# Kernel optimization log

Hardware: AMD Instinct MI355X
Metric: run time of the kernel (lower is better)

Reference implementation:

```python
import jax, jax.numpy as jnp
import numpy as np

DIM = 48
HEADS = 4
DIM_HEAD = 16
WS = 800  # window_size
INNER = HEADS * DIM_HEAD  # 64
SCALE = DIM_HEAD ** -0.5


def setup_inputs() -> dict:
    key = jax.random.key(0)
    k1, k2, k3, k4, k5 = jax.random.split(key, 5)
    b, n = 4, 6400
    x1 = jax.random.normal(k1, (b, n, DIM), dtype=jnp.float32)
    x2 = jax.random.normal(k2, (b, n, DIM), dtype=jnp.float32)
    # to_qkv: Linear(dim, inner*3, bias=False) -> weight [3*inner, dim] (torch layout)
    Wqkv = jax.random.normal(k3, (3 * INNER, DIM), dtype=jnp.float32) * (DIM ** -0.5)
    # to_out: Linear(inner, dim) with bias (project_out is True since heads=4, dim_head=16 != dim)
    Wout = jax.random.normal(k4, (DIM, INNER), dtype=jnp.float32) * (INNER ** -0.5)
    bout = jax.random.normal(k5, (DIM,), dtype=jnp.float32) * 0.01
    return {"x1": x1, "x2": x2, "Wqkv": Wqkv, "Wout": Wout, "bout": bout}


def _windowed_attn(x, Wqkv):
    # x: [b, n, c] with n divisible by WS -> independent full attention per window
    b, n, c = x.shape
    nw = n // WS
    xw = x.reshape(b, nw, WS, c)
    # Rearrange 'b n (head dim_head)' with head=HEADS on 3*inner dim, then chunk(3)
    # => layout along last axis is (heads, 3, dim_head)
    qkv = jnp.einsum('bwic,oc->bwio', xw, Wqkv).reshape(b, nw, WS, HEADS, 3, DIM_HEAD)
    q, k, v = qkv[..., 0, :], qkv[..., 1, :], qkv[..., 2, :]  # [b,nw,ws,h,dh]
    dots = jnp.einsum('bwihd,bwjhd->bwhij', q, k) * SCALE      # [b,nw,h,ws,ws]
    attn = jax.nn.softmax(dots, axis=-1)
    out = jnp.einsum('bwhij,bwjhd->bwihd', attn, v)            # [b,nw,ws,h,dh]
    return out.reshape(b, n, INNER)


def reference(x1, x2, Wqkv, Wout, bout):
    o1 = _windowed_attn(x1, Wqkv) @ Wout.T + bout
    o2 = _windowed_attn(x2, Wqkv) @ Wout.T + bout
    return o1 + o2
```

## Files before the change

### kernel.cpp

```cpp
#include <hip/hip_runtime.h>
#include <cstddef>

typedef __attribute__((ext_vector_type(8))) short short8;
typedef __attribute__((ext_vector_type(16))) float f32x16;

#define NB 4
#define NSEQ 6400
#define CDIM 48
#define DHEAD 16
#define WSZ 800
#define NWIN 8
#define INNER 64
#define NROWS 25600
#define NWH 256
#define SCHUNK (WSZ * DHEAD)
#define CHUNK (3 * SCHUNK)
#define QKV_TOTAL (NWH * CHUNK)
#define AO_PER (NROWS * INNER)

static __device__ __forceinline__ uint pkbf(float a, float b) {
  uint r;
  asm("v_cvt_pk_bf16_f32 %0, %1, %2" : "=v"(r) : "v"(a), "v"(b));
  return r;
}
static __device__ __forceinline__ float bf2f(ushort u) {
  return __uint_as_float(((uint)u) << 16);
}

__global__ __launch_bounds__(256) void qkv_mfma(const float* __restrict__ x1,
                                                const float* __restrict__ x2,
                                                const float* __restrict__ Wqkv,
                                                ushort* __restrict__ wsq) {
  const int tid = threadIdx.x;
  const int lane = tid & 63;
  const int wv = tid >> 6;

  __shared__ __align__(16) ushort Wl[18 * 64 * 8];
  __shared__ __align__(16) ushort Obuf[4][6 * 512];

  for (int slot = tid; slot < 1152; slot += 256) {
    const int mtks = slot >> 6, l2 = slot & 63;
    const int mt = mtks / 3, ks = mtks % 3;
    const int o = mt * 32 + (l2 & 31);
    const int c0 = ks * 16 + (l2 >> 5) * 8;
    const float sc = ((o % CDIM) < DHEAD) ? 0.25f : 1.0f;
    const float4* p = reinterpret_cast<const float4*>(Wqkv + (size_t)o * CDIM + c0);
    float4 u = p[0], v = p[1];
    union { uint q[4]; short8 s; } t;
    t.q[0] = pkbf(u.x * sc, u.y * sc); t.q[1] = pkbf(u.z * sc, u.w * sc);
    t.q[2] = pkbf(v.x * sc, v.y * sc); t.q[3] = pkbf(v.z * sc, v.w * sc);
    *reinterpret_cast<short8*>(Wl + (size_t)slot * 8) = t.s;
  }
  __syncthreads();

  const int task = blockIdx.x * 4 + wv;
  const int batch = task >> 1;
  const int mh = task & 1;
  const int e = batch / 800;
  const int rb = (batch % 800) * 32;
  const float* __restrict__ x = e ? x2 : x1;

  const int rl = lane & 31;
  const int lg = lane >> 5;
  const int row = rb + rl;

  short8 bf[3];
#pragma unroll
  for (int ks = 0; ks < 3; ++ks) {
    const float4* p =
        reinterpret_cast<const float4*>(x + (size_t)row * CDIM + ks * 16 + lg * 8);
    float4 u = p[0], v = p[1];
    union { uint q[4]; short8 s; } t;
    t.q[0] = pkbf(u.x, u.y); t.q[1] = pkbf(u.z, u.w);
    t.q[2] = pkbf(v.x, v.y); t.q[3] = pkbf(v.z, v.w);
    bf[ks] = t.s;
  }

  const int b = rb / NSEQ;
  const int i0 = rb % NSEQ;
  const int wi = i0 / WSZ;
  const int iwb = i0 % WSZ;
  const int whb = ((e * NB + b) * NWIN + wi) * 4;

#pragma unroll
  for (int mt = mh * 3; mt < mh * 3 + 3; ++mt) {
    const int obase = mt * 32;
    short8 wf0 = *reinterpret_cast<const short8*>(Wl + ((mt * 3 + 0) * 64 + lane) * 8);
    short8 wf1 = *reinterpret_cast<const short8*>(Wl + ((mt * 3 + 1) * 64 + lane) * 8);
    short8 wf2 = *reinterpret_cast<const short8*>(Wl + ((mt * 3 + 2) * 64 + lane) * 8);

    f32x16 acc;
#pragma unroll
    for (int r = 0; r < 16; ++r) acc[r] = 0.f;
    acc = __builtin_amdgcn_mfma_f32_32x32x16_bf16(wf0, bf[0], acc, 0, 0, 0);
    acc = __builtin_amdgcn_mfma_f32_32x32x16_bf16(wf1, bf[1], acc, 0, 0, 0);
    acc = __builtin_amdgcn_mfma_f32_32x32x16_bf16(wf2, bf[2], acc, 0, 0, 0);

#pragma unroll
    for (int q = 0; q < 4; ++q) {
      const int op = obase + q * 8 + 4 * lg - mh * 96;
      const int g2 = op >> 4;
      const int d0 = op & 15;
      uint2 pk;
      pk.x = pkbf(acc[4 * q + 0], acc[4 * q + 1]);
      pk.y = pkbf(acc[4 * q + 2], acc[4 * q + 3]);
      *reinterpret_cast<uint2*>(&Obuf[wv][g2 * 512 + rl * 16 + d0]) = pk;
    }
  }

#pragma unroll
  for (int g2 = 0; g2 < 6; ++g2) {
    const int g = mh * 6 + g2;
    const int h = g / 3, s = g % 3;
    short8 val = *reinterpret_cast<const short8*>(&Obuf[wv][g2 * 512 + lane * 8]);
    *reinterpret_cast<short8*>(wsq + (size_t)(whb + h) * CHUNK + s * SCHUNK +
                               (size_t)iwb * DHEAD + lane * 8) = val;
  }
}

#define JC 160
#define NCH 5
#define VROW 168
#define VSL (17 * VROW)

__global__ __launch_bounds__(320) void attn_mfma(const ushort* __restrict__ wsq,
                                                 ushort* __restrict__ ao) {
  const int tid = threadIdx.x;
  const int lane = tid & 63;
  const int wv = tid >> 6;
  const int bid = blockIdx.x;
  const int wh = bid & (NWH - 1);
  const int sub = bid >> 8;
  const int qtile = sub * 5 + wv;

  const ushort* __restrict__ Qg = wsq + (size_t)wh * CHUNK;
  const ushort* __restrict__ Kg = Qg + SCHUNK;
  const ushort* __restrict__ Vg = Kg + SCHUNK;

  __shared__ __align__(16) ushort Vs[2][VSL];

  const int vj = tid % 160;
  const int vhalf = tid / 160;

  short8 vreg = *reinterpret_cast<const short8*>(Vg + (size_t)vj * DHEAD + vhalf * 8);

  if (tid < JC) {
    Vs[0][16 * VROW + tid] = 0x3F80;
    Vs[1][16 * VROW + tid] = 0x3F80;
  }

#pragma unroll
  for (int u = 0; u < 8; ++u)
    Vs[0][(vhalf * 8 + u) * VROW + vj] = (ushort)vreg[u];

  vreg = *reinterpret_cast<const short8*>(Vg + (size_t)(JC + vj) * DHEAD + vhalf * 8);

  short8 qf = *reinterpret_cast<const short8*>(
      Qg + (size_t)(qtile * 32 + (lane & 31)) * DHEAD + (lane >> 5) * 8);

  __syncthreads();

  f32x16 sinit;
#pragma unroll
  for (int r = 0; r < 16; ++r) sinit[r] = -8.0f;
  f32x16 accO;
#pragma unroll
  for (int r = 0; r < 16; ++r) accO[r] = 0.f;

  const int n31 = lane & 31;
  const int lg = lane >> 5;
  const int vrow = (n31 <= 16) ? n31 : (n31 & 15);
  const ushort* __restrict__ kfb = Kg + (size_t)n31 * DHEAD + lg * 8;

  for (int ch = 0; ch < NCH; ++ch) {
    const ushort* __restrict__ Vc = Vs[ch & 1];
#pragma unroll
    for (int jl = 0; jl < 5; ++jl) {
      short8 kf = *reinterpret_cast<const short8*>(
          kfb + (size_t)(ch * JC + jl * 32) * DHEAD);
      f32x16 st = __builtin_amdgcn_mfma_f32_32x32x16_bf16(kf, qf, sinit, 0, 0, 0);

      float p[16];
#pragma unroll
      for (int r = 0; r < 16; ++r) p[r] = __expf(st[r]);

      uint x0, x1, y0, y1;
      asm("v_cvt_pk_bf16_f32 %0, %1, %2" : "=v"(x0) : "v"(p[0]), "v"(p[1]));
      asm("v_cvt_pk_bf16_f32 %0, %1, %2" : "=v"(x1) : "v"(p[2]), "v"(p[3]));
      asm("v_cvt_pk_bf16_f32 %0, %1, %2" : "=v"(y0) : "v"(p[4]), "v"(p[5]));
      asm("v_cvt_pk_bf16_f32 %0, %1, %2" : "=v"(y1) : "v"(p[6]), "v"(p[7]));
      asm("v_permlane32_swap_b32 %0, %1" : "+v"(x0), "+v"(y0));
      asm("v_permlane32_swap_b32 %0, %1" : "+v"(x1), "+v"(y1));
      union { uint u[4]; short8 s; } pa0;
      pa0.u[0] = x0; pa0.u[1] = x1; pa0.u[2] = y0; pa0.u[3] = y1;

      uint z0, z1, w0, w1;
      asm("v_cvt_pk_bf16_f32 %0, %1, %2" : "=v"(z0) : "v"(p[8]), "v"(p[9]));
      asm("v_cvt_pk_bf16_f32 %0, %1, %2" : "=v"(z1) : "v"(p[10]), "v"(p[11]));
      asm("v_cvt_pk_bf16_f32 %0, %1, %2" : "=v"(w0) : "v"(p[12]), "v"(p[13]));
      asm("v_cvt_pk_bf16_f32 %0, %1, %2" : "=v"(w1) : "v"(p[14]), "v"(p[15]));
      asm("v_permlane32_swap_b32 %0, %1" : "+v"(z0), "+v"(w0));
      asm("v_permlane32_swap_b32 %0, %1" : "+v"(z1), "+v"(w1));
      union { uint u[4]; short8 s; } pa1;
      pa1.u[0] = z0; pa1.u[1] = z1; pa1.u[2] = w0; pa1.u[3] = w1;

      short8 vf0 = *reinterpret_cast<const short8*>(Vc + vrow * VROW + jl * 32 + lg * 8);
      short8 vf1 = *reinterpret_cast<const short8*>(Vc + vrow * VROW + jl * 32 + 16 + lg * 8);

      accO = __builtin_amdgcn_mfma_f32_32x32x16_bf16(pa0.s, vf0, accO, 0, 0, 0);
      accO = __builtin_amdgcn_mfma_f32_32x32x16_bf16(pa1.s, vf1, accO, 0, 0, 0);
    }
    if (ch + 1 < NCH) {
      __syncthreads();
      const int nxt = (ch + 1) & 1;
#pragma unroll
      for (int u = 0; u < 8; ++u)
        Vs[nxt][(vhalf * 8 + u) * VROW + vj] = (ushort)vreg[u];
      if (ch + 2 < NCH) {
        vreg = *reinterpret_cast<const short8*>(
            Vg + (size_t)((ch + 2) * JC + vj) * DHEAD + vhalf * 8);
      }
      __syncthreads();
    }
  }

  const int h = wh & 3;
  const int w = (wh >> 2) & 7;
  const int b = (wh >> 5) & 3;
  const int e = wh >> 7;
  const size_t rowbase =
      (size_t)e * NROWS + (size_t)b * NSEQ + (size_t)w * WSZ + (size_t)qtile * 32;
  const int src = 16 + 32 * lg;

#pragma unroll
  for (int r = 0; r < 16; ++r) {
    float den = __shfl(accO[r], src);
    if (n31 < 16) {
      int i = (r & 3) + 8 * (r >> 2) + 4 * lg;
      float val = accO[r] * __builtin_amdgcn_rcpf(den);
      ao[(rowbase + i) * INNER + h * DHEAD + n31] = (ushort)pkbf(val, val);
    }
  }
}

#define OSTR 76
__global__ __launch_bounds__(192) void out_proj(const ushort* __restrict__ ao_all,
                                                const float* __restrict__ Wout,
                                                const float* __restrict__ bout,
                                                float* __restrict__ out) {
  const int tid = threadIdx.x;
  const int row0 = blockIdx.x * 64;

  __shared__ float aos[64 * OSTR];

  const ushort* __restrict__ a1 = ao_all;
  const ushort* __restrict__ a2 = ao_all + (size_t)AO_PER;

  for (int idx = tid; idx < 64 * 8; idx += 192) {
    const int r = idx >> 3, c = idx & 7;
    const size_t g = (size_t)(row0 + r) * INNER + c * 8;
    short8 u = *reinterpret_cast<const short8*>(a1 + g);
    short8 v = *reinterpret_cast<const short8*>(a2 + g);
    float4 s0, s1;
    s0.x = bf2f((ushort)u[0]) + bf2f((ushort)v[0]);
    s0.y = bf2f((ushort)u[1]) + bf2f((ushort)v[1]);
    s0.z = bf2f((ushort)u[2]) + bf2f((ushort)v[2]);
    s0.w = bf2f((ushort)u[3]) + bf2f((ushort)v[3]);
    s1.x = bf2f((ushort)u[4]) + bf2f((ushort)v[4]);
    s1.y = bf2f((ushort)u[5]) + bf2f((ushort)v[5]);
    s1.z = bf2f((ushort)u[6]) + bf2f((ushort)v[6]);
    s1.w = bf2f((ushort)u[7]) + bf2f((ushort)v[7]);
    *reinterpret_cast<float4*>(aos + r * OSTR + c * 8) = s0;
    *reinterpret_cast<float4*>(aos + r * OSTR + c * 8 + 4) = s1;
  }

  const int j = tid % 48;
  const int rq = tid / 48;

  float wreg[INNER];
#pragma unroll
  for (int k4 = 0; k4 < 16; ++k4) {
    float4 wv4 = reinterpret_cast<const float4*>(Wout + (size_t)j * INNER)[k4];
    wreg[k4 * 4 + 0] = wv4.x; wreg[k4 * 4 + 1] = wv4.y;
    wreg[k4 * 4 + 2] = wv4.z; wreg[k4 * 4 + 3] = wv4.w;
  }
  const float bj = 2.0f * bout[j];

  __syncthreads();

  for (int r16 = 0; r16 < 16; ++r16) {
    const int r = rq * 16 + r16;
    float a0 = 0.f, a1v = 0.f, a2v = 0.f, a3 = 0.f;
#pragma unroll
    for (int kk = 0; kk < 16; ++kk) {
      const int k4 = (kk + rq * 4) & 15;
      float4 av = *reinterpret_cast<const float4*>(aos + r * OSTR + k4 * 4);
      a0 = fmaf(av.x, wreg[k4 * 4 + 0], a0);
      a1v = fmaf(av.y, wreg[k4 * 4 + 1], a1v);
      a2v = fmaf(av.z, wreg[k4 * 4 + 2], a2v);
      a3 = fmaf(av.w, wreg[k4 * 4 + 3], a3);
    }
    out[(size_t)(row0 + r) * CDIM + j] = (a0 + a1v) + (a2v + a3) + bj;
  }
}

extern "C" void kernel_launch(void* const* d_in, const int* in_sizes, int n_in,
                              void* d_out, int out_size, void* d_ws,
                              size_t ws_size, hipStream_t stream) {
  const float* x1 = (const float*)d_in[0];
  const float* x2 = (const float*)d_in[1];
  const float* Wqkv = (const float*)d_in[2];
  const float* Wout = (const float*)d_in[3];
  const float* bout = (const float*)d_in[4];
  float* out = (float*)d_out;
  ushort* wsq = (ushort*)d_ws;
  ushort* ao = wsq + QKV_TOTAL;

  qkv_mfma<<<dim3(800), dim3(256), 0, stream>>>(x1, x2, Wqkv, wsq);
  attn_mfma<<<dim3(1280), dim3(320), 0, stream>>>(wsq, ao);
  out_proj<<<dim3(400), dim3(192), 0, stream>>>(ao, Wout, bout, out);
}
```

Measured before the change: 65.74 us.

## Rewrite output projection using bf16 MFMA with LDS-staged coalesced stores

Replaces the scalar FP32 FMA output projection with a kernel that converts Wout to bf16 in shared memory and uses 32x32x16 bf16 MFMA instructions. The two attention branches are summed by accumulating both into the same accumulator. Results are staged in LDS per wave and written out with coalesced float4 stores. This aims to cut ALU and LDS cost in the final GEMM, at the price of rounding the weights to bf16.

```diff
diff --git a/kernel.cpp b/kernel.cpp
--- a/kernel.cpp
+++ b/kernel.cpp
@@ -243,64 +243,79 @@
   }
 }
 
-#define OSTR 76
-__global__ __launch_bounds__(192) void out_proj(const ushort* __restrict__ ao_all,
+__global__ __launch_bounds__(256) void out_mfma(const ushort* __restrict__ ao_all,
                                                 const float* __restrict__ Wout,
                                                 const float* __restrict__ bout,
                                                 float* __restrict__ out) {
   const int tid = threadIdx.x;
-  const int row0 = blockIdx.x * 64;
-
-  __shared__ float aos[64 * OSTR];
+  const int lane = tid & 63;
+  const int wv = tid >> 6;
+
+  __shared__ __align__(16) ushort Wlo[8 * 64 * 8];
+  __shared__ __align__(16) float Obuf[4][32 * 48];
+
+  for (int slot = tid; slot < 512; slot += 256) {
+    const int mtks = slot >> 6, l2 = slot & 63;
+    const int mt = mtks >> 2, ks = mtks & 3;
+    int o = mt * 32 + (l2 & 31);
+    if (o > 47) o = 47;
+    const int c0 = ks * 16 + (l2 >> 5) * 8;
+    const float4* p = reinterpret_cast<const float4*>(Wout + (size_t)o * INNER + c0);
+    float4 u = p[0], v = p[1];
+    union { uint q[4]; short8 s; } t;
+    t.q[0] = pkbf(u.x, u.y); t.q[1] = pkbf(u.z, u.w);
+    t.q[2] = pkbf(v.x, v.y); t.q[3] = pkbf(v.z, v.w);
+    *reinterpret_cast<short8*>(Wlo + (size_t)slot * 8) = t.s;
+  }
+  __syncthreads();
+
+  const int rb = (blockIdx.x * 4 + wv) * 32;
+  const int rl = lane & 31;
+  const int lg = lane >> 5;
 
   const ushort* __restrict__ a1 = ao_all;
   const ushort* __restrict__ a2 = ao_all + (size_t)AO_PER;
 
-  for (int idx = tid; idx < 64 * 8; idx += 192) {
-    const int r = idx >> 3, c = idx & 7;
-    const size_t g = (size_t)(row0 + r) * INNER + c * 8;
-    short8 u = *reinterpret_cast<const short8*>(a1 + g);
-    short8 v = *reinterpret_cast<const short8*>(a2 + g);
-    float4 s0, s1;
-    s0.x = bf2f((ushort)u[0]) + bf2f((ushort)v[0]);
-    s0.y = bf2f((ushort)u[1]) + bf2f((ushort)v[1]);
-    s0.z = bf2f((ushort)u[2]) + bf2f((ushort)v[2]);
-    s0.w = bf2f((ushort)u[3]) + bf2f((ushort)v[3]);
-    s1.x = bf2f((ushort)u[4]) + bf2f((ushort)v[4]);
-    s1.y = bf2f((ushort)u[5]) + bf2f((ushort)v[5]);
-    s1.z = bf2f((ushort)u[6]) + bf2f((ushort)v[6]);
-    s1.w = bf2f((ushort)u[7]) + bf2f((ushort)v[7]);
-    *reinterpret_cast<float4*>(aos + r * OSTR + c * 8) = s0;
-    *reinterpret_cast<float4*>(aos + r * OSTR + c * 8 + 4) = s1;
-  }
-
-  const int j = tid % 48;
-  const int rq = tid / 48;
-
-  float wreg[INNER];
-#pragma unroll
-  for (int k4 = 0; k4 < 16; ++k4) {
-    float4 wv4 = reinterpret_cast<const float4*>(Wout + (size_t)j * INNER)[k4];
-    wreg[k4 * 4 + 0] = wv4.x; wreg[k4 * 4 + 1] = wv4.y;
-    wreg[k4 * 4 + 2] = wv4.z; wreg[k4 * 4 + 3] = wv4.w;
-  }
-  const float bj = 2.0f * bout[j];
-
-  __syncthreads();
-
-  for (int r16 = 0; r16 < 16; ++r16) {
-    const int r = rq * 16 + r16;
-    float a0 = 0.f, a1v = 0.f, a2v = 0.f, a3 = 0.f;
-#pragma unroll
-    for (int kk = 0; kk < 16; ++kk) {
-      const int k4 = (kk + rq * 4) & 15;
-      float4 av = *reinterpret_cast<const float4*>(aos + r * OSTR + k4 * 4);
-      a0 = fmaf(av.x, wreg[k4 * 4 + 0], a0);
-      a1v = fmaf(av.y, wreg[k4 * 4 + 1], a1v);
-      a2v = fmaf(av.z, wreg[k4 * 4 + 2], a2v);
-      a3 = fmaf(av.w, wreg[k4 * 4 + 3], a3);
-    }
-    out[(size_t)(row0 + r) * CDIM + j] = (a0 + a1v) + (a2v + a3) + bj;
+  short8 b1[4], b2[4];
+#pragma unroll
+  for (int ks = 0; ks < 4; ++ks) {
+    b1[ks] = *reinterpret_cast<const short8*>(
+        a1 + (size_t)(rb + rl) * INNER + ks * 16 + lg * 8);
+    b2[ks] = *reinterpret_cast<const short8*>(
+        a2 + (size_t)(rb + rl) * INNER + ks * 16 + lg * 8);
+  }
+
+#pragma unroll
+  for (int mt = 0; mt < 2; ++mt) {
+    f32x16 acc;
+#pragma unroll
+    for (int r = 0; r < 16; ++r) acc[r] = 0.f;
+#pragma unroll
+    for (int ks = 0; ks < 4; ++ks) {
+      short8 wf = *reinterpret_cast<const short8*>(
+          Wlo + ((size_t)(mt * 4 + ks) * 64 + lane) * 8);
+      acc = __builtin_amdgcn_mfma_f32_32x32x16_bf16(wf, b1[ks], acc, 0, 0, 0);
+      acc = __builtin_amdgcn_mfma_f32_32x32x16_bf16(wf, b2[ks], acc, 0, 0, 0);
+    }
+#pragma unroll
+    for (int q = 0; q < 4; ++q) {
+      const int op = mt * 32 + q * 8 + 4 * lg;
+      if (op < CDIM) {
+        float4 bb = *reinterpret_cast<const float4*>(bout + op);
+        float4 val;
+        val.x = acc[4 * q + 0] + 2.0f * bb.x;
+        val.y = acc[4 * q + 1] + 2.0f * bb.y;
+        val.z = acc[4 * q + 2] + 2.0f * bb.z;
+        val.w = acc[4 * q + 3] + 2.0f * bb.w;
+        *reinterpret_cast<float4*>(&Obuf[wv][rl * CDIM + op]) = val;
+      }
+    }
+  }
+
+#pragma unroll
+  for (int it = 0; it < 6; ++it) {
+    float4 v = *reinterpret_cast<const float4*>(&Obuf[wv][it * 256 + lane * 4]);
+    *reinterpret_cast<float4*>(out + (size_t)rb * CDIM + it * 256 + lane * 4) = v;
   }
 }
 
@@ -318,5 +333,5 @@
 
   qkv_mfma<<<dim3(800), dim3(256), 0, stream>>>(x1, x2, Wqkv, wsq);
   attn_mfma<<<dim3(1280), dim3(320), 0, stream>>>(wsq, ao);
-  out_proj<<<dim3(400), dim3(192), 0, stream>>>(ao, Wout, bout, out);
-}
+  out_mfma<<<dim3(200), dim3(256), 0, stream>>>(ao, Wout, bout, out);
+}
```

After: 53.89 us (median of 2 runs). -18.0%, faster.
